# Optimization experiments

Measured on AMD Instinct MI355X. Metric: run time of the kernel, lower is better.

## Reference

```python
import jax, jax.numpy as jnp
import numpy as np

E = 8          # num_experts
TOP_K = 2
D = 1024       # hidden_size
I_MOE = 1024   # moe_intermediate_size (per-expert)
I_SH = 4096    # intermediate_size (shared expert)


def setup_inputs() -> dict:
    key = jax.random.key(0)
    ks = jax.random.split(key, 9)
    s = 0.02
    return {
        "hidden_states": jax.random.normal(ks[0], (2, 4096, D), dtype=jnp.float32),
        "gate_w": jax.random.normal(ks[1], (D, E), dtype=jnp.float32) * s,
        "eg": jax.random.normal(ks[2], (E, D, I_MOE), dtype=jnp.float32) * s,  # gate_proj per expert
        "eu": jax.random.normal(ks[3], (E, D, I_MOE), dtype=jnp.float32) * s,  # up_proj per expert
        "ed": jax.random.normal(ks[4], (E, I_MOE, D), dtype=jnp.float32) * s,  # down_proj per expert
        "sg": jax.random.normal(ks[5], (D, I_SH), dtype=jnp.float32) * s,
        "su": jax.random.normal(ks[6], (D, I_SH), dtype=jnp.float32) * s,
        "sd": jax.random.normal(ks[7], (I_SH, D), dtype=jnp.float32) * s,
        "shared_gate_w": jax.random.normal(ks[8], (D, 1), dtype=jnp.float32) * s,
    }


def _swiglu(x, wg, wu, wd):
    # down_proj(silu(gate_proj(x)) * up_proj(x))
    return (jax.nn.silu(x @ wg) * (x @ wu)) @ wd


def reference(hidden_states, gate_w, eg, eu, ed, sg, su, sd, shared_gate_w):
    B, S, Dm = hidden_states.shape
    x = hidden_states.reshape(-1, Dm)                     # [T, D]

    router_logits = x @ gate_w                            # [T, E]
    probs = jax.nn.softmax(router_logits.astype(jnp.float32), axis=-1)
    topw, topi = jax.lax.top_k(probs, TOP_K)              # [T, K]
    topw = topw / jnp.clip(jnp.sum(topw, axis=-1, keepdims=True), 1e-6)
    topw = topw.astype(x.dtype)

    # combine[t, e] = routing weight of expert e for token t (0 if unselected)
    combine = jnp.sum(jax.nn.one_hot(topi, E, dtype=x.dtype) * topw[..., None], axis=1)  # [T, E]

    out = jnp.zeros_like(x)
    for e in range(E):  # fixed small expert loop (structurally distinct weights)
        out = out + combine[:, e:e + 1] * _swiglu(x, eg[e], eu[e], ed[e])

    shared = _swiglu(x, sg, su, sd)
    shared_gate = jax.nn.sigmoid(x @ shared_gate_w)       # [T, 1]
    out = out + shared_gate * shared

    return out.reshape(B, S, Dm), router_logits
```

## Files before the change

### kernel.cpp

```cpp
#include <hip/hip_runtime.h>
#include <hip/hip_bf16.h>
#include <stdint.h>

#define T_TOK 8192
#define DDIM 1024
#define NEXP 8
#define IMOE 1024
#define ISH 4096
#define BK 64
#define PADTOT 17408

typedef __attribute__((ext_vector_type(8))) short short8;
typedef __attribute__((ext_vector_type(8))) __bf16 bf16x8;
typedef __attribute__((ext_vector_type(4))) float floatx4;

__device__ __forceinline__ unsigned short f2bf(float f) {
  union { float f; unsigned u; } v; v.f = f;
  unsigned r = v.u + 0x7fffu + ((v.u >> 16) & 1u);
  return (unsigned short)(r >> 16);
}

__device__ __forceinline__ floatx4 mfma16(short8 a, short8 b, floatx4 c) {
  return __builtin_amdgcn_mfma_f32_16x16x32_bf16(
      __builtin_bit_cast(bf16x8, a), __builtin_bit_cast(bf16x8, b), c, 0, 0, 0);
}

__device__ __forceinline__ void gload16(const void* g, void* l) {
  __builtin_amdgcn_global_load_lds((const __attribute__((address_space(1))) void*)g,
                                   (__attribute__((address_space(3))) void*)l, 16, 0, 0);
}

__device__ __forceinline__ void xcd_swz(int id, int gm, int gn, int& m, int& n) {
  int cpx = (gm * gn) >> 3;
  int wg = (id & 7) * cpx + (id >> 3);
  int g = wg >> 6, r = wg & 63;
  int gpr = gn >> 3;
  m = ((g / gpr) << 3) | (r >> 3);
  n = ((g % gpr) << 3) | (r & 7);
}



__global__ void k_cast(const float* __restrict__ src, unsigned short* __restrict__ dst, int n) {
  int i = (blockIdx.x * blockDim.x + threadIdx.x) * 4;
  if (i < n) {
    float4 v = *(const float4*)(src + i);
    ushort4 o;
    o.x = f2bf(v.x); o.y = f2bf(v.y); o.z = f2bf(v.z); o.w = f2bf(v.w);
    *(ushort4*)(dst + i) = o;
  }
}

__global__ void k_transpose_cast(const float* __restrict__ src, unsigned short* __restrict__ dst,
                                 int R, int C) {
  __shared__ float tile[32][33];
  int b = blockIdx.z;
  int c0 = blockIdx.x * 32, r0 = blockIdx.y * 32;
  const float* s = src + (size_t)b * R * C;
  unsigned short* d = dst + (size_t)b * R * C;
  int tx = threadIdx.x, ty = threadIdx.y;
#pragma unroll
  for (int j = 0; j < 32; j += 8)
    tile[ty + j][tx] = s[(size_t)(r0 + ty + j) * C + c0 + tx];
  __syncthreads();
#pragma unroll
  for (int j = 0; j < 32; j += 8)
    d[(size_t)(c0 + ty + j) * R + r0 + tx] = f2bf(tile[tx][ty + j]);
}


__global__ void k_router(const float* __restrict__ x, const float* __restrict__ gw,
                         const float* __restrict__ sgw, float* __restrict__ logits_out,
                         int* __restrict__ topi, float* __restrict__ topw,
                         float* __restrict__ sgate) {
  int wave = threadIdx.x >> 6;
  int lane = threadIdx.x & 63;
  int t = blockIdx.x * 4 + wave;
  const float* xr = x + (size_t)t * DDIM;
  float acc[9];
#pragma unroll
  for (int j = 0; j < 9; j++) acc[j] = 0.f;
  for (int d = lane; d < DDIM; d += 64) {
    float xv = xr[d];
    const float* g = gw + d * 8;
    float4 g0 = *(const float4*)g;
    float4 g1 = *(const float4*)(g + 4);
    acc[0] += xv * g0.x; acc[1] += xv * g0.y; acc[2] += xv * g0.z; acc[3] += xv * g0.w;
    acc[4] += xv * g1.x; acc[5] += xv * g1.y; acc[6] += xv * g1.z; acc[7] += xv * g1.w;
    acc[8] += xv * sgw[d];
  }
#pragma unroll
  for (int off = 32; off > 0; off >>= 1) {
#pragma unroll
    for (int j = 0; j < 9; j++) acc[j] += __shfl_xor(acc[j], off);
  }
  if (lane == 0) {
#pragma unroll
    for (int j = 0; j < 8; j++) logits_out[t * 8 + j] = acc[j];
    int i0 = 0;
#pragma unroll
    for (int j = 1; j < 8; j++) if (acc[j] > acc[i0]) i0 = j;
    int i1 = -1;
#pragma unroll
    for (int j = 0; j < 8; j++) {
      if (j == i0) continue;
      if (i1 < 0 || acc[j] > acc[i1]) i1 = j;
    }
    float e1 = expf(acc[i1] - acc[i0]);
    float inv = 1.f / (1.f + e1);
    topi[t * 2] = i0; topi[t * 2 + 1] = i1;
    topw[t * 2] = inv; topw[t * 2 + 1] = e1 * inv;
    sgate[t] = 1.f / (1.f + expf(-acc[8]));
  }
}

__global__ void k_hist(const int* __restrict__ topi, int* __restrict__ blockhist) {
  __shared__ int h[NEXP];
  if (threadIdx.x < NEXP) h[threadIdx.x] = 0;
  __syncthreads();
  int i = blockIdx.x * 256 + threadIdx.x;
  atomicAdd(&h[topi[i]], 1);
  __syncthreads();
  if (threadIdx.x < NEXP) blockhist[blockIdx.x * NEXP + threadIdx.x] = h[threadIdx.x];
}

__global__ void k_offsets(const int* __restrict__ blockhist, int* __restrict__ pseg,
                          int* __restrict__ rcnt, int* __restrict__ blockbase) {
  if (threadIdx.x == 0) {
    int tot[NEXP];
#pragma unroll
    for (int e = 0; e < NEXP; e++) tot[e] = 0;
    for (int b = 0; b < 64; b++)
      for (int e = 0; e < NEXP; e++) {
        blockbase[b * NEXP + e] = tot[e];
        tot[e] += blockhist[b * NEXP + e];
      }
    int s = 0;
    for (int e = 0; e < NEXP; e++) {
      rcnt[e] = tot[e];
      pseg[e] = s;
      s += (tot[e] + 127) & ~127;
    }
    pseg[NEXP] = s;
    for (int b = 0; b < 64; b++)
      for (int e = 0; e < NEXP; e++) blockbase[b * NEXP + e] += pseg[e];
  }
}

__global__ void k_scatter(const int* __restrict__ topi, const float* __restrict__ topw,
                          const int* __restrict__ blockbase,
                          int* __restrict__ ptok, float* __restrict__ pw) {
  __shared__ int cur[NEXP];
  if (threadIdx.x < NEXP) cur[threadIdx.x] = blockbase[blockIdx.x * NEXP + threadIdx.x];
  __syncthreads();
  int i = blockIdx.x * 256 + threadIdx.x;
  int e = topi[i];
  int pos = atomicAdd(&cur[e], 1);
  ptok[pos] = i >> 1;
  pw[pos] = topw[i];
}

__global__ __launch_bounds__(256, 4) void k_gu_shared(
    const unsigned short* __restrict__ Xb,
    const unsigned short* __restrict__ BgT,
    const unsigned short* __restrict__ BuT,
    unsigned short* __restrict__ H)
{
  int bm, bn;
  xcd_swz(blockIdx.x, 64, 64, bm, bn);
  const int tm0 = bm * 128;
  const int tn0 = bn * 64;

  __shared__ __align__(16) unsigned short As[128 * BK];
  __shared__ __align__(16) unsigned short Bgs[64 * BK];
  __shared__ __align__(16) unsigned short Bus[64 * BK];

  const int tid = threadIdx.x;
  const int wave = tid >> 6, lane = tid & 63;
  const int wm = wave & 1, wn = wave >> 1;
  const int quad = lane >> 4, l16 = lane & 15;
  const int srow = lane >> 3;
  const int scol = ((lane & 7) ^ srow) * 8;

  floatx4 accg[4][2] = {};
  floatx4 accu[4][2] = {};

  for (int k0 = 0; k0 < DDIM; k0 += BK) {
#pragma unroll
    for (int s = 0; s < 4; s++) {
      int rb = (wave * 4 + s) * 8;
      gload16(Xb + (size_t)(tm0 + rb + srow) * DDIM + k0 + scol, As + rb * BK);
    }
#pragma unroll
    for (int s = 0; s < 2; s++) {
      int rb = (wave * 2 + s) * 8;
      gload16(BgT + (size_t)(tn0 + rb + srow) * DDIM + k0 + scol, Bgs + rb * BK);
      gload16(BuT + (size_t)(tn0 + rb + srow) * DDIM + k0 + scol, Bus + rb * BK);
    }
    __syncthreads();
#pragma unroll
    for (int ks = 0; ks < BK; ks += 32) {
      short8 af[4], bg[2], bu[2];
#pragma unroll
      for (int f = 0; f < 4; f++) {
        int r = wm * 64 + f * 16 + l16;
        af[f] = *(const short8*)(As + r * BK + ((((ks >> 3) + quad) ^ (r & 7)) << 3));
      }
#pragma unroll
      for (int f = 0; f < 2; f++) {
        int r = wn * 32 + f * 16 + l16;
        int off = r * BK + ((((ks >> 3) + quad) ^ (r & 7)) << 3);
        bg[f] = *(const short8*)(Bgs + off);
        bu[f] = *(const short8*)(Bus + off);
      }
#pragma unroll
      for (int fm = 0; fm < 4; fm++)
#pragma unroll
        for (int fn = 0; fn < 2; fn++) {
          accg[fm][fn] = mfma16(af[fm], bg[fn], accg[fm][fn]);
          accu[fm][fn] = mfma16(af[fm], bu[fn], accu[fm][fn]);
        }
    }
    __syncthreads();
  }
#pragma unroll
  for (int fm = 0; fm < 4; fm++)
#pragma unroll
    for (int reg = 0; reg < 4; reg++) {
      int r = tm0 + wm * 64 + fm * 16 + quad * 4 + reg;
#pragma unroll
      for (int fn = 0; fn < 2; fn++) {
        int c = tn0 + wn * 32 + fn * 16 + l16;
        float g = accg[fm][fn][reg];
        float u = accu[fm][fn][reg];
        float h = (g / (1.f + __expf(-g))) * u;
        H[(size_t)r * ISH + c] = f2bf(h);
      }
    }
}

__global__ __launch_bounds__(256, 4) void k_gu_expert(
    const unsigned short* __restrict__ Xb,
    const unsigned short* __restrict__ EgT,
    const unsigned short* __restrict__ EuT,
    const int* __restrict__ pseg,
    const int* __restrict__ ptok,
    unsigned short* __restrict__ Hp)
{
  int bm, bn;
  xcd_swz(blockIdx.x, PADTOT / 128, 16, bm, bn);
  const int m0 = bm * 128;
  if (m0 >= pseg[NEXP]) return;
  int e = 0;
#pragma unroll
  for (int j = 1; j < NEXP; j++) if (m0 >= pseg[j]) e = j;

  __shared__ __align__(16) unsigned short As[128 * BK];
  __shared__ __align__(16) unsigned short Bgs[64 * BK];
  __shared__ __align__(16) unsigned short Bus[64 * BK];

  const int tn0 = bn * 64;
  const int tid = threadIdx.x;
  const int wave = tid >> 6, lane = tid & 63;
  const int wm = wave & 1, wn = wave >> 1;
  const int quad = lane >> 4, l16 = lane & 15;
  const int srow = lane >> 3;
  const int scol = ((lane & 7) ^ srow) * 8;

  const unsigned short* Bg = EgT + (size_t)e * IMOE * DDIM;
  const unsigned short* Bu = EuT + (size_t)e * IMOE * DDIM;

  const unsigned short* ArowP[4];
#pragma unroll
  for (int s = 0; s < 4; s++) {
    int tok = ptok[m0 + (wave * 4 + s) * 8 + srow];
    if (tok < 0 || tok >= T_TOK) tok = 0;
    ArowP[s] = Xb + (size_t)tok * DDIM + scol;
  }

  floatx4 accg[4][2] = {};
  floatx4 accu[4][2] = {};

  for (int k0 = 0; k0 < DDIM; k0 += BK) {
#pragma unroll
    for (int s = 0; s < 4; s++) {
      int rb = (wave * 4 + s) * 8;
      gload16(ArowP[s] + k0, As + rb * BK);
    }
#pragma unroll
    for (int s = 0; s < 2; s++) {
      int rb = (wave * 2 + s) * 8;
      gload16(Bg + (size_t)(tn0 + rb + srow) * DDIM + k0 + scol, Bgs + rb * BK);
      gload16(Bu + (size_t)(tn0 + rb + srow) * DDIM + k0 + scol, Bus + rb * BK);
    }
    __syncthreads();
#pragma unroll
    for (int ks = 0; ks < BK; ks += 32) {
      short8 af[4], bg[2], bu[2];
#pragma unroll
      for (int f = 0; f < 4; f++) {
        int r = wm * 64 + f * 16 + l16;
        af[f] = *(const short8*)(As + r * BK + ((((ks >> 3) + quad) ^ (r & 7)) << 3));
      }
#pragma unroll
      for (int f = 0; f < 2; f++) {
        int r = wn * 32 + f * 16 + l16;
        int off = r * BK + ((((ks >> 3) + quad) ^ (r & 7)) << 3);
        bg[f] = *(const short8*)(Bgs + off);
        bu[f] = *(const short8*)(Bus + off);
      }
#pragma unroll
      for (int fm = 0; fm < 4; fm++)
#pragma unroll
        for (int fn = 0; fn < 2; fn++) {
          accg[fm][fn] = mfma16(af[fm], bg[fn], accg[fm][fn]);
          accu[fm][fn] = mfma16(af[fm], bu[fn], accu[fm][fn]);
        }
    }
    __syncthreads();
  }
#pragma unroll
  for (int fm = 0; fm < 4; fm++)
#pragma unroll
    for (int reg = 0; reg < 4; reg++) {
      int r = m0 + wm * 64 + fm * 16 + quad * 4 + reg;
#pragma unroll
      for (int fn = 0; fn < 2; fn++) {
        int c = tn0 + wn * 32 + fn * 16 + l16;
        float g = accg[fm][fn][reg];
        float u = accu[fm][fn][reg];
        Hp[(size_t)r * IMOE + c] = f2bf((g / (1.f + __expf(-g))) * u);
      }
    }
}

__global__ __launch_bounds__(256, 4) void k_down_shared(
    const unsigned short* __restrict__ Hsh,
    const unsigned short* __restrict__ SdT,
    const float* __restrict__ sgate,
    float* __restrict__ out)
{
  __shared__ __align__(16) unsigned short As[128 * BK];
  __shared__ __align__(16) unsigned short Bs[128 * BK];

  int bm, bn;
  xcd_swz(blockIdx.x, 64, 8, bm, bn);
  const int tm0 = bm * 128;
  const int tn0 = bn * 128;
  const int tid = threadIdx.x;
  const int wave = tid >> 6, lane = tid & 63;
  const int wm = wave & 1, wn = wave >> 1;
  const int quad = lane >> 4, l16 = lane & 15;
  const int srow = lane >> 3;
  const int scol = ((lane & 7) ^ srow) * 8;

  floatx4 acc[4][4] = {};

  for (int k0 = 0; k0 < ISH; k0 += BK) {
#pragma unroll
    for (int s = 0; s < 4; s++) {
      int rb = (wave * 4 + s) * 8;
      gload16(Hsh + (size_t)(tm0 + rb + srow) * ISH + k0 + scol, As + rb * BK);
      gload16(SdT + (size_t)(tn0 + rb + srow) * ISH + k0 + scol, Bs + rb * BK);
    }
    __syncthreads();
#pragma unroll
    for (int ks = 0; ks < BK; ks += 32) {
      short8 af[4], bfr[4];
#pragma unroll
      for (int f = 0; f < 4; f++) {
        int ra = wm * 64 + f * 16 + l16;
        int rb2 = wn * 64 + f * 16 + l16;
        af[f] = *(const short8*)(As + ra * BK + ((((ks >> 3) + quad) ^ (ra & 7)) << 3));
        bfr[f] = *(const short8*)(Bs + rb2 * BK + ((((ks >> 3) + quad) ^ (rb2 & 7)) << 3));
      }
#pragma unroll
      for (int fm = 0; fm < 4; fm++)
#pragma unroll
        for (int fn = 0; fn < 4; fn++)
          acc[fm][fn] = mfma16(af[fm], bfr[fn], acc[fm][fn]);
    }
    __syncthreads();
  }
#pragma unroll
  for (int fm = 0; fm < 4; fm++)
#pragma unroll
    for (int reg = 0; reg < 4; reg++) {
      int r = tm0 + wm * 64 + fm * 16 + quad * 4 + reg;
      float gt = sgate[r];
#pragma unroll
      for (int fn = 0; fn < 4; fn++) {
        int c = tn0 + wn * 64 + fn * 16 + l16;
        out[(size_t)r * DDIM + c] = gt * acc[fm][fn][reg];
      }
    }
}

__global__ __launch_bounds__(256, 4) void k_down_expert(
    const unsigned short* __restrict__ Hp,
    const unsigned short* __restrict__ EdT,
    const int* __restrict__ pseg,
    const int* __restrict__ rcnt,
    const int* __restrict__ ptok,
    const float* __restrict__ pw,
    float* __restrict__ out)
{
  int bm, bn;
  xcd_swz(blockIdx.x, PADTOT / 128, 8, bm, bn);
  const int m0 = bm * 128;
  if (m0 >= pseg[NEXP]) return;
  int e = 0;
#pragma unroll
  for (int j = 1; j < NEXP; j++) if (m0 >= pseg[j]) e = j;
  const int sbase = pseg[e];
  const int cnt = rcnt[e];

  __shared__ __align__(16) unsigned short As[128 * BK];
  __shared__ __align__(16) unsigned short Bs[128 * BK];

  const int tn0 = bn * 128;
  const int tid = threadIdx.x;
  const int wave = tid >> 6, lane = tid & 63;
  const int wm = wave & 1, wn = wave >> 1;
  const int quad = lane >> 4, l16 = lane & 15;
  const int srow = lane >> 3;
  const int scol = ((lane & 7) ^ srow) * 8;

  const unsigned short* B = EdT + (size_t)e * IMOE * DDIM;

  floatx4 acc[4][4] = {};

  for (int k0 = 0; k0 < IMOE; k0 += BK) {
#pragma unroll
    for (int s = 0; s < 4; s++) {
      int rb = (wave * 4 + s) * 8;
      gload16(Hp + (size_t)(m0 + rb + srow) * IMOE + k0 + scol, As + rb * BK);
      gload16(B + (size_t)(tn0 + rb + srow) * IMOE + k0 + scol, Bs + rb * BK);
    }
    __syncthreads();
#pragma unroll
    for (int ks = 0; ks < BK; ks += 32) {
      short8 af[4], bfr[4];
#pragma unroll
      for (int f = 0; f < 4; f++) {
        int ra = wm * 64 + f * 16 + l16;
        int rb2 = wn * 64 + f * 16 + l16;
        af[f] = *(const short8*)(As + ra * BK + ((((ks >> 3) + quad) ^ (ra & 7)) << 3));
        bfr[f] = *(const short8*)(Bs + rb2 * BK + ((((ks >> 3) + quad) ^ (rb2 & 7)) << 3));
      }
#pragma unroll
      for (int fm = 0; fm < 4; fm++)
#pragma unroll
        for (int fn = 0; fn < 4; fn++)
          acc[fm][fn] = mfma16(af[fm], bfr[fn], acc[fm][fn]);
    }
    __syncthreads();
  }
#pragma unroll
  for (int fm = 0; fm < 4; fm++)
#pragma unroll
    for (int reg = 0; reg < 4; reg++) {
      int grow = m0 + wm * 64 + fm * 16 + quad * 4 + reg;
      if (grow - sbase < cnt) {
        int t = ptok[grow];
        float w = pw[grow];
#pragma unroll
        for (int fn = 0; fn < 4; fn++) {
          int c = tn0 + wn * 64 + fn * 16 + l16;
          atomicAdd(&out[(size_t)t * DDIM + c], w * acc[fm][fn][reg]);
        }
      }
    }
}


extern "C" void kernel_launch(void* const* d_in, const int* in_sizes, int n_in,
                              void* d_out, int out_size, void* d_ws, size_t ws_size,
                              hipStream_t stream) {
  const float* x   = (const float*)d_in[0];
  const float* gw  = (const float*)d_in[1];
  const float* eg  = (const float*)d_in[2];
  const float* eu  = (const float*)d_in[3];
  const float* ed  = (const float*)d_in[4];
  const float* sg  = (const float*)d_in[5];
  const float* su  = (const float*)d_in[6];
  const float* sd  = (const float*)d_in[7];
  const float* sgw = (const float*)d_in[8];

  float* out    = (float*)d_out;
  float* logits = out + (size_t)T_TOK * DDIM;

  char* ws = (char*)d_ws;
  unsigned short* xb   = (unsigned short*)(ws + 0);
  unsigned short* egT  = (unsigned short*)(ws + 16777216);
  unsigned short* euT  = (unsigned short*)(ws + 33554432);
  unsigned short* edT  = (unsigned short*)(ws + 50331648);
  unsigned short* sgT  = (unsigned short*)(ws + 67108864);
  unsigned short* suT  = (unsigned short*)(ws + 75497472);
  unsigned short* sdT  = (unsigned short*)(ws + 83886080);
  unsigned short* hsh  = (unsigned short*)(ws + 92274688);
  unsigned short* hp   = (unsigned short*)(ws + 159383552);
  int*   topi      = (int*)  (ws + 195035136);
  float* topw      = (float*)(ws + 195100672);
  float* sgate     = (float*)(ws + 195166208);
  int*   ptok      = (int*)  (ws + 195198976);
  float* pw        = (float*)(ws + 195268608);
  int*   blockhist = (int*)  (ws + 195338240);
  int*   blockbase = (int*)  (ws + 195340288);
  int*   pseg      = (int*)  (ws + 195342336);
  int*   rcnt      = (int*)  (ws + 195342400);

  k_cast<<<8192, 256, 0, stream>>>(x, xb, T_TOK * DDIM);
  k_transpose_cast<<<dim3(32, 32, 8), dim3(32, 8), 0, stream>>>(eg, egT, DDIM, IMOE);
  k_transpose_cast<<<dim3(32, 32, 8), dim3(32, 8), 0, stream>>>(eu, euT, DDIM, IMOE);
  k_transpose_cast<<<dim3(32, 32, 8), dim3(32, 8), 0, stream>>>(ed, edT, IMOE, DDIM);
  k_transpose_cast<<<dim3(128, 32, 1), dim3(32, 8), 0, stream>>>(sg, sgT, DDIM, ISH);
  k_transpose_cast<<<dim3(128, 32, 1), dim3(32, 8), 0, stream>>>(su, suT, DDIM, ISH);
  k_transpose_cast<<<dim3(32, 128, 1), dim3(32, 8), 0, stream>>>(sd, sdT, ISH, DDIM);

  k_router<<<T_TOK / 4, 256, 0, stream>>>(x, gw, sgw, logits, topi, topw, sgate);
  k_hist<<<64, 256, 0, stream>>>(topi, blockhist);
  k_offsets<<<1, 64, 0, stream>>>(blockhist, pseg, rcnt, blockbase);
  k_scatter<<<64, 256, 0, stream>>>(topi, topw, blockbase, ptok, pw);

  k_gu_expert<<<(PADTOT / 128) * 16, 256, 0, stream>>>(xb, egT, euT, pseg, ptok, hp);
  k_gu_shared<<<64 * 64, 256, 0, stream>>>(xb, sgT, suT, hsh);
  k_down_shared<<<64 * 8, 256, 0, stream>>>(hsh, sdT, sgate, out);
  k_down_expert<<<(PADTOT / 128) * 8, 256, 0, stream>>>(hp, edT, pseg, rcnt, ptok, pw, out);

  (void)in_sizes; (void)n_in; (void)out_size; (void)ws_size;
}
```

Before: 647.9 us.

## Fuse cast into router, merge transpose launches, parallelize offsets, drop shared swizzle

Folds the bf16 cast of activations into the router kernel, which already reads x, so one full pass over the input is dropped. The six transpose-cast launches become three, and the single-thread prefix scan in k_offsets becomes a per-expert parallel scan. The XCD swizzle is removed from the shared-expert GEMMs in favour of a plain 2D grid, and the shared GEMMs now launch before the expert ones. Dropping the swizzle may reduce L2 locality for the shared GEMMs.

```diff
diff --git a/kernel.cpp b/kernel.cpp
--- a/kernel.cpp
+++ b/kernel.cpp
@@ -30,7 +30,7 @@
                                    (__attribute__((address_space(3))) void*)l, 16, 0, 0);
 }
 
-__device__ __forceinline__ void xcd_swz(int id, int gm, int gn, int& m, int& n) {
+__device__ __forceinline__ void swz_ms(int id, int gm, int gn, int& m, int& n) {
   int cpx = (gm * gn) >> 3;
   int wg = (id & 7) * cpx + (id >> 3);
   int g = wg >> 6, r = wg & 63;
@@ -41,23 +41,10 @@
 
 
 
-__global__ void k_cast(const float* __restrict__ src, unsigned short* __restrict__ dst, int n) {
-  int i = (blockIdx.x * blockDim.x + threadIdx.x) * 4;
-  if (i < n) {
-    float4 v = *(const float4*)(src + i);
-    ushort4 o;
-    o.x = f2bf(v.x); o.y = f2bf(v.y); o.z = f2bf(v.z); o.w = f2bf(v.w);
-    *(ushort4*)(dst + i) = o;
-  }
-}
-
-__global__ void k_transpose_cast(const float* __restrict__ src, unsigned short* __restrict__ dst,
-                                 int R, int C) {
+__device__ __forceinline__ void tr_cast_body(const float* __restrict__ s,
+                                             unsigned short* __restrict__ d, int R, int C) {
   __shared__ float tile[32][33];
-  int b = blockIdx.z;
   int c0 = blockIdx.x * 32, r0 = blockIdx.y * 32;
-  const float* s = src + (size_t)b * R * C;
-  unsigned short* d = dst + (size_t)b * R * C;
   int tx = threadIdx.x, ty = threadIdx.y;
 #pragma unroll
   for (int j = 0; j < 32; j += 8)
@@ -66,22 +53,43 @@
 #pragma unroll
   for (int j = 0; j < 32; j += 8)
     d[(size_t)(c0 + ty + j) * R + r0 + tx] = f2bf(tile[tx][ty + j]);
+}
+
+__global__ void k_tr_experts(const float* __restrict__ eg, const float* __restrict__ eu,
+                             const float* __restrict__ ed, unsigned short* __restrict__ egT,
+                             unsigned short* __restrict__ euT, unsigned short* __restrict__ edT) {
+  int z = blockIdx.z, sel = z >> 3, b = z & 7;
+  const float* s = (sel == 0 ? eg : sel == 1 ? eu : ed) + (size_t)b * 1024 * 1024;
+  unsigned short* d = (sel == 0 ? egT : sel == 1 ? euT : edT) + (size_t)b * 1024 * 1024;
+  tr_cast_body(s, d, 1024, 1024);
+}
+
+__global__ void k_tr_su(const float* __restrict__ sg, const float* __restrict__ su,
+                        unsigned short* __restrict__ sgT, unsigned short* __restrict__ suT) {
+  if (blockIdx.z == 0) tr_cast_body(sg, sgT, DDIM, ISH);
+  else                 tr_cast_body(su, suT, DDIM, ISH);
+}
+
+__global__ void k_tr_sd(const float* __restrict__ sd, unsigned short* __restrict__ sdT) {
+  tr_cast_body(sd, sdT, ISH, DDIM);
 }
 
 
 __global__ void k_router(const float* __restrict__ x, const float* __restrict__ gw,
                          const float* __restrict__ sgw, float* __restrict__ logits_out,
                          int* __restrict__ topi, float* __restrict__ topw,
-                         float* __restrict__ sgate) {
+                         float* __restrict__ sgate, unsigned short* __restrict__ xb) {
   int wave = threadIdx.x >> 6;
   int lane = threadIdx.x & 63;
   int t = blockIdx.x * 4 + wave;
   const float* xr = x + (size_t)t * DDIM;
+  unsigned short* xbr = xb + (size_t)t * DDIM;
   float acc[9];
 #pragma unroll
   for (int j = 0; j < 9; j++) acc[j] = 0.f;
   for (int d = lane; d < DDIM; d += 64) {
     float xv = xr[d];
+    xbr[d] = f2bf(xv);
     const float* g = gw + d * 8;
     float4 g0 = *(const float4*)g;
     float4 g1 = *(const float4*)(g + 4);
@@ -126,24 +134,35 @@
 
 __global__ void k_offsets(const int* __restrict__ blockhist, int* __restrict__ pseg,
                           int* __restrict__ rcnt, int* __restrict__ blockbase) {
-  if (threadIdx.x == 0) {
-    int tot[NEXP];
-#pragma unroll
-    for (int e = 0; e < NEXP; e++) tot[e] = 0;
-    for (int b = 0; b < 64; b++)
-      for (int e = 0; e < NEXP; e++) {
-        blockbase[b * NEXP + e] = tot[e];
-        tot[e] += blockhist[b * NEXP + e];
-      }
+  __shared__ int h[64 * NEXP];
+  __shared__ int tot[NEXP], ps[NEXP + 1];
+  int t = threadIdx.x;
+#pragma unroll
+  for (int j = 0; j < 8; j++) h[j * 64 + t] = blockhist[j * 64 + t];
+  __syncthreads();
+  if (t < NEXP) {
     int s = 0;
-    for (int e = 0; e < NEXP; e++) {
-      rcnt[e] = tot[e];
-      pseg[e] = s;
-      s += (tot[e] + 127) & ~127;
-    }
-    pseg[NEXP] = s;
-    for (int b = 0; b < 64; b++)
-      for (int e = 0; e < NEXP; e++) blockbase[b * NEXP + e] += pseg[e];
+    for (int b = 0; b < 64; b++) {
+      int v = h[b * NEXP + t];
+      h[b * NEXP + t] = s;
+      s += v;
+    }
+    tot[t] = s;
+    rcnt[t] = s;
+  }
+  __syncthreads();
+  if (t == 0) {
+    int s = 0;
+    for (int e = 0; e < NEXP; e++) { ps[e] = s; s += (tot[e] + 127) & ~127; }
+    ps[NEXP] = s;
+#pragma unroll
+    for (int e = 0; e <= NEXP; e++) pseg[e] = ps[e];
+  }
+  __syncthreads();
+#pragma unroll
+  for (int j = 0; j < 8; j++) {
+    int idx = j * 64 + t;
+    blockbase[idx] = h[idx] + ps[idx & 7];
   }
 }
 
@@ -159,6 +178,7 @@
   ptok[pos] = i >> 1;
   pw[pos] = topw[i];
 }
+
 
 __global__ __launch_bounds__(256, 4) void k_gu_shared(
     const unsigned short* __restrict__ Xb,
@@ -166,10 +186,8 @@
     const unsigned short* __restrict__ BuT,
     unsigned short* __restrict__ H)
 {
-  int bm, bn;
-  xcd_swz(blockIdx.x, 64, 64, bm, bn);
-  const int tm0 = bm * 128;
-  const int tn0 = bn * 64;
+  const int tm0 = blockIdx.x * 128;
+  const int tn0 = blockIdx.y * 64;
 
   __shared__ __align__(16) unsigned short As[128 * BK];
   __shared__ __align__(16) unsigned short Bgs[64 * BK];
@@ -248,7 +266,7 @@
     unsigned short* __restrict__ Hp)
 {
   int bm, bn;
-  xcd_swz(blockIdx.x, PADTOT / 128, 16, bm, bn);
+  swz_ms(blockIdx.x, PADTOT / 128, 16, bm, bn);
   const int m0 = bm * 128;
   if (m0 >= pseg[NEXP]) return;
   int e = 0;
@@ -343,10 +361,8 @@
   __shared__ __align__(16) unsigned short As[128 * BK];
   __shared__ __align__(16) unsigned short Bs[128 * BK];
 
-  int bm, bn;
-  xcd_swz(blockIdx.x, 64, 8, bm, bn);
-  const int tm0 = bm * 128;
-  const int tn0 = bn * 128;
+  const int tm0 = blockIdx.x * 128;
+  const int tn0 = blockIdx.y * 128;
   const int tid = threadIdx.x;
   const int wave = tid >> 6, lane = tid & 63;
   const int wm = wave & 1, wn = wave >> 1;
@@ -406,7 +422,7 @@
     float* __restrict__ out)
 {
   int bm, bn;
-  xcd_swz(blockIdx.x, PADTOT / 128, 8, bm, bn);
+  swz_ms(blockIdx.x, PADTOT / 128, 8, bm, bn);
   const int m0 = bm * 128;
   if (m0 >= pseg[NEXP]) return;
   int e = 0;
@@ -508,24 +524,20 @@
   int*   blockhist = (int*)  (ws + 195338240);
   int*   blockbase = (int*)  (ws + 195340288);
   int*   pseg      = (int*)  (ws + 195342336);
-  int*   rcnt      = (int*)  (ws + 195342400);
-
-  k_cast<<<8192, 256, 0, stream>>>(x, xb, T_TOK * DDIM);
-  k_transpose_cast<<<dim3(32, 32, 8), dim3(32, 8), 0, stream>>>(eg, egT, DDIM, IMOE);
-  k_transpose_cast<<<dim3(32, 32, 8), dim3(32, 8), 0, stream>>>(eu, euT, DDIM, IMOE);
-  k_transpose_cast<<<dim3(32, 32, 8), dim3(32, 8), 0, stream>>>(ed, edT, IMOE, DDIM);
-  k_transpose_cast<<<dim3(128, 32, 1), dim3(32, 8), 0, stream>>>(sg, sgT, DDIM, ISH);
-  k_transpose_cast<<<dim3(128, 32, 1), dim3(32, 8), 0, stream>>>(su, suT, DDIM, ISH);
-  k_transpose_cast<<<dim3(32, 128, 1), dim3(32, 8), 0, stream>>>(sd, sdT, ISH, DDIM);
-
-  k_router<<<T_TOK / 4, 256, 0, stream>>>(x, gw, sgw, logits, topi, topw, sgate);
+  int*   rcnt     = (int*)  (ws + 195342400);
+
+  k_router<<<T_TOK / 4, 256, 0, stream>>>(x, gw, sgw, logits, topi, topw, sgate, xb);
+  k_tr_experts<<<dim3(32, 32, 24), dim3(32, 8), 0, stream>>>(eg, eu, ed, egT, euT, edT);
+  k_tr_su<<<dim3(128, 32, 2), dim3(32, 8), 0, stream>>>(sg, su, sgT, suT);
+  k_tr_sd<<<dim3(32, 128, 1), dim3(32, 8), 0, stream>>>(sd, sdT);
+
   k_hist<<<64, 256, 0, stream>>>(topi, blockhist);
   k_offsets<<<1, 64, 0, stream>>>(blockhist, pseg, rcnt, blockbase);
   k_scatter<<<64, 256, 0, stream>>>(topi, topw, blockbase, ptok, pw);
 
+  k_gu_shared<<<dim3(64, 64), 256, 0, stream>>>(xb, sgT, suT, hsh);
+  k_down_shared<<<dim3(64, 8), 256, 0, stream>>>(hsh, sdT, sgate, out);
   k_gu_expert<<<(PADTOT / 128) * 16, 256, 0, stream>>>(xb, egT, euT, pseg, ptok, hp);
-  k_gu_shared<<<64 * 64, 256, 0, stream>>>(xb, sgT, suT, hsh);
-  k_down_shared<<<64 * 8, 256, 0, stream>>>(hsh, sdT, sgate, out);
   k_down_expert<<<(PADTOT / 128) * 8, 256, 0, stream>>>(hp, edT, pseg, rcnt, ptok, pw, out);
 
   (void)in_sizes; (void)n_in; (void)out_size; (void)ws_size;
```

Measured after the change: 617.8 us. 1.05x faster.
